# Optimization experiments

Measured on AMD Instinct MI355X. Metric: run time of the kernel, lower is better.

## Reference

```python
import jax, jax.numpy as jnp
import numpy as np

B, N, H_DIM, E_DIM, M_DIM = 16, 128, 128, 64, 128


def setup_inputs() -> dict:
    key = jax.random.key(0)
    k_h, k_e, k_adj, k_w, k_b = jax.random.split(key, 5)
    h = jax.random.normal(k_h, (B, N, H_DIM), dtype=jnp.float32)
    e = jax.random.normal(k_e, (B, N, N, E_DIM), dtype=jnp.float32)
    # binary adjacency mask stored as float (multiplied elementwise, as in torch)
    adj = (jax.random.uniform(k_adj, (B, N, N)) < 0.3).astype(jnp.float32)
    in_dim = 2 * H_DIM + E_DIM
    # nn.Linear default init: U(-1/sqrt(fan_in), 1/sqrt(fan_in))
    bound = 1.0 / np.sqrt(in_dim)
    W = jax.random.uniform(k_w, (in_dim, M_DIM), minval=-bound, maxval=bound, dtype=jnp.float32)
    b = jax.random.uniform(k_b, (M_DIM,), minval=-bound, maxval=bound, dtype=jnp.float32)
    return {"h": h, "e": e, "adj": adj, "W": W, "b": b}


def reference(h, e, adj, W, b):
    # torch: cat([h_j (unsqueeze(1) repeat), h_i (unsqueeze(2) repeat), e], -1) @ W + b, then * adj
    # Split the concat-linear into three matmuls (same math, no O(N^2 * (2h+e)) cat tensor):
    hd = h.shape[-1]
    W1 = W[:hd]          # acts on h_repeat_1 = h[b, j]
    W2 = W[hd:2 * hd]    # acts on h_repeat_2 = h[b, i]
    W3 = W[2 * hd:]      # acts on e[b, i, j]
    t1 = jnp.einsum('bjd,dm->bjm', h, W1)[:, None, :, :]   # broadcast over i
    t2 = jnp.einsum('bid,dm->bim', h, W2)[:, :, None, :]   # broadcast over j
    t3 = jnp.einsum('bije,em->bijm', e, W3)
    m = (t1 + t2 + t3 + b) * adj[..., None]                 # [B, N, N, M_DIM]
    return m
```

## Files before the change

### kernel.cpp

```cpp
#include <hip/hip_runtime.h>
#include <hip/hip_bf16.h>

#define NB 16
#define NN 128
#define HD 128
#define ED 64
#define MD 128

typedef float f32x4 __attribute__((ext_vector_type(4)));

__global__ __launch_bounds__(128, 8) void prep_kernel(
    const float* __restrict__ h, const float* __restrict__ W,
    const float* __restrict__ bias,
    float* __restrict__ hw1, float* __restrict__ t2pb)
{
    __shared__ float hs[HD];
    const int row = blockIdx.x;
    const int m   = threadIdx.x;

    hs[m] = h[(size_t)row * HD + m];
    __syncthreads();

    float a1 = 0.f, a2 = 0.f;
    const float* W1p = W + m;
    const float* W2p = W + (size_t)HD * MD + m;
#pragma unroll 8
    for (int d = 0; d < HD; ++d) {
        const float hv = hs[d];
        a1 = fmaf(hv, W1p[(size_t)d * MD], a1);
        a2 = fmaf(hv, W2p[(size_t)d * MD], a2);
    }
    hw1 [(size_t)row * MD + m] = a1;
    t2pb[(size_t)row * MD + m] = a2 + bias[m];
}

__global__ __launch_bounds__(512, 4) void msg_kernel(
    const float* __restrict__ e, const float* __restrict__ adj,
    const float* __restrict__ W, const float* __restrict__ hw1,
    const float* __restrict__ t2pb, float* __restrict__ out)
{
    __shared__ float smem[16384];
    float4* __restrict__ eq = (float4*)smem;
    float4* __restrict__ wq = (float4*)(smem + 8192);

    const int bx   = blockIdx.x;
    const int tid  = threadIdx.x;
    const int w    = __builtin_amdgcn_readfirstlane(tid >> 6);
    const int lane = tid & 63;

    const float4* __restrict__ e4  = (const float4*)(e + (size_t)bx * NN * ED);
    const float4* __restrict__ W3q = (const float4*)(W + (size_t)(2 * HD) * MD);

#pragma unroll
    for (int it = 0; it < 4; ++it) {
        const int idx = tid + it * 512;
        const int j   = idx >> 4;
        const int kq  = idx & 15;
        eq[16 * j + (kq ^ (j & 7))] = e4[idx];
        wq[idx] = W3q[idx];
    }
    __syncthreads();

    const int jhalf = w & 1;
    const int mq4   = w >> 1;
    const int j     = jhalf * 64 + lane;
    const int jx    = j & 7;
    const int ebase = 16 * j;
    const int wbase = 8 * mq4;

    float acc[32];
#pragma unroll
    for (int i = 0; i < 32; ++i) acc[i] = 0.f;

#pragma unroll 2
    for (int q = 0; q < 16; ++q) {
        const float4 ev = eq[ebase + (q ^ jx)];
#pragma unroll
        for (int kk = 0; kk < 4; ++kk) {
            const float evk = (kk == 0) ? ev.x : (kk == 1) ? ev.y
                             : (kk == 2) ? ev.z : ev.w;
            const float4* __restrict__ wrow = wq + 32 * (4 * q + kk) + wbase;
#pragma unroll
            for (int p = 0; p < 8; ++p) {
                const float4 wv = wrow[p];
                acc[4 * p + 0] = fmaf(evk, wv.x, acc[4 * p + 0]);
                acc[4 * p + 1] = fmaf(evk, wv.y, acc[4 * p + 1]);
                acc[4 * p + 2] = fmaf(evk, wv.z, acc[4 * p + 2]);
                acc[4 * p + 3] = fmaf(evk, wv.w, acc[4 * p + 3]);
            }
        }
    }

    float4* __restrict__ tq = wq;
    const float*  __restrict__ adjrow = adj  + (size_t)bx * NN;
    const float4* __restrict__ hw1b   = (const float4*)(hw1 + (size_t)(bx >> 7) * NN * MD);
    const float4* __restrict__ t2row  = (const float4*)(t2pb + (size_t)bx * MD);
    f32x4*        __restrict__ outb   = (f32x4*)(out + (size_t)bx * NN * MD);

#pragma unroll
    for (int h = 0; h < 2; ++h) {
        __syncthreads();
        if (jhalf == h) {
            const int lx = lane & 7;
#pragma unroll
            for (int p = 0; p < 8; ++p) {
                const int qm = wbase + p;
                tq[32 * lane + (qm ^ lx)] =
                    make_float4(acc[4 * p + 0], acc[4 * p + 1],
                                acc[4 * p + 2], acc[4 * p + 3]);
            }
        }
        __syncthreads();
#pragma unroll
        for (int it = 0; it < 4; ++it) {
            const int t4 = tid + it * 512;
            const int jl = t4 >> 5;
            const int mq = t4 & 31;
            const int jg = h * 64 + jl;
            const float4 v  = tq[32 * jl + (mq ^ (jl & 7))];
            const float4 h1 = hw1b[(size_t)jg * 32 + mq];
            const float4 t2 = t2row[mq];
            const float  a  = adjrow[jg];
            f32x4 r;
            r.x = (v.x + h1.x + t2.x) * a;
            r.y = (v.y + h1.y + t2.y) * a;
            r.z = (v.z + h1.z + t2.z) * a;
            r.w = (v.w + h1.w + t2.w) * a;
            __builtin_nontemporal_store(r, outb + (size_t)jg * 32 + mq);
        }
    }
}

extern "C" void kernel_launch(void* const* d_in, const int* in_sizes, int n_in,
                              void* d_out, int out_size, void* d_ws, size_t ws_size,
                              hipStream_t stream)
{
    const float* h    = (const float*)d_in[0];
    const float* e    = (const float*)d_in[1];
    const float* adj  = (const float*)d_in[2];
    const float* W    = (const float*)d_in[3];
    const float* bias = (const float*)d_in[4];
    float* out = (float*)d_out;

    float* hw1  = (float*)d_ws;
    float* t2pb = hw1 + (size_t)NB * NN * MD;

    prep_kernel<<<dim3(NB * NN), dim3(128), 0, stream>>>(h, W, bias, hw1, t2pb);
    msg_kernel <<<dim3(NB * NN), dim3(512), 0, stream>>>(e, adj, W, hw1, t2pb, out);
}
```

Measured before the change: 239.0 us.

## Halve block size, register-block two j rows per thread, load e directly from global

The message kernel now runs 256 threads per block. Each thread accumulates two j rows (j and j+64) and reuses each LDS W3 read across both. The e tile is no longer staged in shared memory: each thread reads its float4s straight from global, which cuts LDS to 32 KB and the W3 read traffic per FMA. The cost is 64 accumulators per thread, raising register pressure and possibly occupancy limits, plus strided uncoalesced global loads of e.

Result: no change. 239.4 us (+0.2%).

```diff
diff --git a/kernel.cpp b/kernel.cpp
--- a/kernel.cpp
+++ b/kernel.cpp
@@ -34,14 +34,12 @@
     t2pb[(size_t)row * MD + m] = a2 + bias[m];
 }
 
-__global__ __launch_bounds__(512, 4) void msg_kernel(
+__global__ __launch_bounds__(256, 4) void msg_kernel(
     const float* __restrict__ e, const float* __restrict__ adj,
     const float* __restrict__ W, const float* __restrict__ hw1,
     const float* __restrict__ t2pb, float* __restrict__ out)
 {
-    __shared__ float smem[16384];
-    float4* __restrict__ eq = (float4*)smem;
-    float4* __restrict__ wq = (float4*)(smem + 8192);
+    __shared__ float4 smem[2048];
 
     const int bx   = blockIdx.x;
     const int tid  = threadIdx.x;
@@ -52,46 +50,45 @@
     const float4* __restrict__ W3q = (const float4*)(W + (size_t)(2 * HD) * MD);
 
 #pragma unroll
-    for (int it = 0; it < 4; ++it) {
-        const int idx = tid + it * 512;
-        const int j   = idx >> 4;
-        const int kq  = idx & 15;
-        eq[16 * j + (kq ^ (j & 7))] = e4[idx];
-        wq[idx] = W3q[idx];
-    }
+    for (int it = 0; it < 8; ++it)
+        smem[tid + it * 256] = W3q[tid + it * 256];
     __syncthreads();
 
-    const int jhalf = w & 1;
-    const int mq4   = w >> 1;
-    const int j     = jhalf * 64 + lane;
-    const int jx    = j & 7;
-    const int ebase = 16 * j;
-    const int wbase = 8 * mq4;
+    const int wbase = 8 * w;
 
-    float acc[32];
+    float acc[2][32];
 #pragma unroll
-    for (int i = 0; i < 32; ++i) acc[i] = 0.f;
+    for (int r = 0; r < 2; ++r)
+#pragma unroll
+        for (int i = 0; i < 32; ++i) acc[r][i] = 0.f;
 
 #pragma unroll 2
     for (int q = 0; q < 16; ++q) {
-        const float4 ev = eq[ebase + (q ^ jx)];
+        const float4 ev0 = e4[lane * 16 + q];
+        const float4 ev1 = e4[(lane + 64) * 16 + q];
 #pragma unroll
         for (int kk = 0; kk < 4; ++kk) {
-            const float evk = (kk == 0) ? ev.x : (kk == 1) ? ev.y
-                             : (kk == 2) ? ev.z : ev.w;
-            const float4* __restrict__ wrow = wq + 32 * (4 * q + kk) + wbase;
+            const float e0 = (kk == 0) ? ev0.x : (kk == 1) ? ev0.y
+                            : (kk == 2) ? ev0.z : ev0.w;
+            const float e1 = (kk == 0) ? ev1.x : (kk == 1) ? ev1.y
+                            : (kk == 2) ? ev1.z : ev1.w;
+            const float4* __restrict__ wrow = smem + 32 * (4 * q + kk) + wbase;
 #pragma unroll
             for (int p = 0; p < 8; ++p) {
                 const float4 wv = wrow[p];
-                acc[4 * p + 0] = fmaf(evk, wv.x, acc[4 * p + 0]);
-                acc[4 * p + 1] = fmaf(evk, wv.y, acc[4 * p + 1]);
-                acc[4 * p + 2] = fmaf(evk, wv.z, acc[4 * p + 2]);
-                acc[4 * p + 3] = fmaf(evk, wv.w, acc[4 * p + 3]);
+                acc[0][4 * p + 0] = fmaf(e0, wv.x, acc[0][4 * p + 0]);
+                acc[0][4 * p + 1] = fmaf(e0, wv.y, acc[0][4 * p + 1]);
+                acc[0][4 * p + 2] = fmaf(e0, wv.z, acc[0][4 * p + 2]);
+                acc[0][4 * p + 3] = fmaf(e0, wv.w, acc[0][4 * p + 3]);
+                acc[1][4 * p + 0] = fmaf(e1, wv.x, acc[1][4 * p + 0]);
+                acc[1][4 * p + 1] = fmaf(e1, wv.y, acc[1][4 * p + 1]);
+                acc[1][4 * p + 2] = fmaf(e1, wv.z, acc[1][4 * p + 2]);
+                acc[1][4 * p + 3] = fmaf(e1, wv.w, acc[1][4 * p + 3]);
             }
         }
     }
 
-    float4* __restrict__ tq = wq;
+    float4* __restrict__ tq = smem;
     const float*  __restrict__ adjrow = adj  + (size_t)bx * NN;
     const float4* __restrict__ hw1b   = (const float4*)(hw1 + (size_t)(bx >> 7) * NN * MD);
     const float4* __restrict__ t2row  = (const float4*)(t2pb + (size_t)bx * MD);
@@ -100,20 +97,20 @@
 #pragma unroll
     for (int h = 0; h < 2; ++h) {
         __syncthreads();
-        if (jhalf == h) {
+        {
             const int lx = lane & 7;
 #pragma unroll
             for (int p = 0; p < 8; ++p) {
                 const int qm = wbase + p;
                 tq[32 * lane + (qm ^ lx)] =
-                    make_float4(acc[4 * p + 0], acc[4 * p + 1],
-                                acc[4 * p + 2], acc[4 * p + 3]);
+                    make_float4(acc[h][4 * p + 0], acc[h][4 * p + 1],
+                                acc[h][4 * p + 2], acc[h][4 * p + 3]);
             }
         }
         __syncthreads();
 #pragma unroll
-        for (int it = 0; it < 4; ++it) {
-            const int t4 = tid + it * 512;
+        for (int it = 0; it < 8; ++it) {
+            const int t4 = tid + it * 256;
             const int jl = t4 >> 5;
             const int mq = t4 & 31;
             const int jg = h * 64 + jl;
@@ -146,5 +143,5 @@
     float* t2pb = hw1 + (size_t)NB * NN * MD;
 
     prep_kernel<<<dim3(NB * NN), dim3(128), 0, stream>>>(h, W, bias, hw1, t2pb);
-    msg_kernel <<<dim3(NB * NN), dim3(512), 0, stream>>>(e, adj, W, hw1, t2pb, out);
+    msg_kernel <<<dim3(NB * NN), dim3(256), 0, stream>>>(e, adj, W, hw1, t2pb, out);
 }
```

## Compute edge projection with split-bf16 MFMA instead of scalar FP32 FMAs

Applied to the files above, without the earlier changes.

The e@W3 product per (b,i) row is moved from scalar FP32 FMAs onto bf16 MFMA instructions. Each FP32 operand is split into a high and a low bf16 part, and three MFMA passes (hi*hi, hi*lo, lo*hi) approximate FP32 accuracy. Half the waves load and pack W3 into LDS while the other half load and pack e, and the epilogue now writes the full tile to LDS once instead of in two halves. The trade-off is that W3 is re-packed in every block and there is some precision loss from dropping the lo*lo term.

After: 209.4 us. -12.4%, faster.

```diff
diff --git a/kernel.cpp b/kernel.cpp
--- a/kernel.cpp
+++ b/kernel.cpp
@@ -8,6 +8,16 @@
 #define MD 128
 
 typedef float f32x4 __attribute__((ext_vector_type(4)));
+typedef short bf16x8 __attribute__((ext_vector_type(8)));
+
+__device__ __forceinline__ unsigned pack_hi(float a, float b) {
+    return (__float_as_uint(a) >> 16) | (__float_as_uint(b) & 0xFFFF0000u);
+}
+__device__ __forceinline__ unsigned pack_lo(float a, float b) {
+    const float ra = a - __uint_as_float(__float_as_uint(a) & 0xFFFF0000u);
+    const float rb = b - __uint_as_float(__float_as_uint(b) & 0xFFFF0000u);
+    return (__float_as_uint(ra) >> 16) | (__float_as_uint(rb) & 0xFFFF0000u);
+}
 
 __global__ __launch_bounds__(128, 8) void prep_kernel(
     const float* __restrict__ h, const float* __restrict__ W,
@@ -39,95 +49,148 @@
     const float* __restrict__ W, const float* __restrict__ hw1,
     const float* __restrict__ t2pb, float* __restrict__ out)
 {
-    __shared__ float smem[16384];
-    float4* __restrict__ eq = (float4*)smem;
-    float4* __restrict__ wq = (float4*)(smem + 8192);
+    __shared__ char smem[65536];
 
     const int bx   = blockIdx.x;
     const int tid  = threadIdx.x;
+    const int lane = tid & 63;
     const int w    = __builtin_amdgcn_readfirstlane(tid >> 6);
-    const int lane = tid & 63;
-
-    const float4* __restrict__ e4  = (const float4*)(e + (size_t)bx * NN * ED);
-    const float4* __restrict__ W3q = (const float4*)(W + (size_t)(2 * HD) * MD);
-
-#pragma unroll
-    for (int it = 0; it < 4; ++it) {
-        const int idx = tid + it * 512;
-        const int j   = idx >> 4;
-        const int kq  = idx & 15;
-        eq[16 * j + (kq ^ (j & 7))] = e4[idx];
-        wq[idx] = W3q[idx];
-    }
-    __syncthreads();
-
-    const int jhalf = w & 1;
-    const int mq4   = w >> 1;
-    const int j     = jhalf * 64 + lane;
-    const int jx    = j & 7;
-    const int ebase = 16 * j;
-    const int wbase = 8 * mq4;
-
-    float acc[32];
-#pragma unroll
-    for (int i = 0; i < 32; ++i) acc[i] = 0.f;
-
-#pragma unroll 2
-    for (int q = 0; q < 16; ++q) {
-        const float4 ev = eq[ebase + (q ^ jx)];
-#pragma unroll
-        for (int kk = 0; kk < 4; ++kk) {
-            const float evk = (kk == 0) ? ev.x : (kk == 1) ? ev.y
-                             : (kk == 2) ? ev.z : ev.w;
-            const float4* __restrict__ wrow = wq + 32 * (4 * q + kk) + wbase;
-#pragma unroll
-            for (int p = 0; p < 8; ++p) {
-                const float4 wv = wrow[p];
-                acc[4 * p + 0] = fmaf(evk, wv.x, acc[4 * p + 0]);
-                acc[4 * p + 1] = fmaf(evk, wv.y, acc[4 * p + 1]);
-                acc[4 * p + 2] = fmaf(evk, wv.z, acc[4 * p + 2]);
-                acc[4 * p + 3] = fmaf(evk, wv.w, acc[4 * p + 3]);
+
+    if (w < 4) {
+        const int m  = tid & 127;
+        const int kh = tid >> 7;
+        const float* __restrict__ W3 = W + (size_t)(2 * HD) * MD;
+        float col[32];
+#pragma unroll
+        for (int k = 0; k < 32; ++k)
+            col[k] = W3[(size_t)(kh * 32 + k) * MD + m];
+        const unsigned swz = (unsigned)((m & 7) << 4);
+#pragma unroll
+        for (int q = 0; q < 4; ++q) {
+            uint4 hi, lo;
+            hi.x = pack_hi(col[8*q+0], col[8*q+1]);
+            hi.y = pack_hi(col[8*q+2], col[8*q+3]);
+            hi.z = pack_hi(col[8*q+4], col[8*q+5]);
+            hi.w = pack_hi(col[8*q+6], col[8*q+7]);
+            lo.x = pack_lo(col[8*q+0], col[8*q+1]);
+            lo.y = pack_lo(col[8*q+2], col[8*q+3]);
+            lo.z = pack_lo(col[8*q+4], col[8*q+5]);
+            lo.w = pack_lo(col[8*q+6], col[8*q+7]);
+            const unsigned off = (unsigned)((m << 7) + (kh << 6) + (q << 4)) ^ swz;
+            *(uint4*)(smem + 32768 + off) = hi;
+            *(uint4*)(smem + 49152 + off) = lo;
+        }
+    } else {
+        const int s = tid - 256;
+        const float4* __restrict__ e4 = (const float4*)(e + (size_t)bx * NN * ED);
+        float4 ev[8];
+#pragma unroll
+        for (int it = 0; it < 8; ++it)
+            ev[it] = e4[it * 256 + s];
+#pragma unroll
+        for (int it = 0; it < 8; ++it) {
+            const int idx = it * 256 + s;
+            const int j   = idx >> 4;
+            const int kq  = idx & 15;
+            const unsigned off =
+                ((unsigned)((j << 7) + (kq << 3))) ^ (unsigned)((j & 7) << 4);
+            uint2 hi, lo;
+            hi.x = pack_hi(ev[it].x, ev[it].y);
+            hi.y = pack_hi(ev[it].z, ev[it].w);
+            lo.x = pack_lo(ev[it].x, ev[it].y);
+            lo.y = pack_lo(ev[it].z, ev[it].w);
+            *(uint2*)(smem + off)         = hi;
+            *(uint2*)(smem + 16384 + off) = lo;
+        }
+    }
+    __syncthreads();
+
+    const int jh  = w & 1;
+    const int mq  = w >> 1;
+    const int jb  = jh * 64;
+    const int mb  = mq * 32;
+    const int l15 = lane & 15;
+    const int g   = lane >> 4;
+
+    f32x4 acc[4][2];
+#pragma unroll
+    for (int jt = 0; jt < 4; ++jt)
+#pragma unroll
+        for (int mt = 0; mt < 2; ++mt)
+            acc[jt][mt] = (f32x4){0.f, 0.f, 0.f, 0.f};
+
+#pragma unroll
+    for (int pass = 0; pass < 3; ++pass) {
+        const int abase = (pass == 2) ? 16384 : 0;
+        const int bbase = (pass == 1) ? 49152 : 32768;
+#pragma unroll
+        for (int kt = 0; kt < 2; ++kt) {
+            bf16x8 a[4], b[2];
+#pragma unroll
+            for (int jt = 0; jt < 4; ++jt) {
+                const int j = jb + jt * 16 + l15;
+                const unsigned off =
+                    ((unsigned)((j << 7) + (kt << 6) + (g << 4)))
+                    ^ (unsigned)((j & 7) << 4);
+                a[jt] = *(const bf16x8*)(smem + abase + off);
             }
-        }
-    }
-
-    float4* __restrict__ tq = wq;
+#pragma unroll
+            for (int mt = 0; mt < 2; ++mt) {
+                const int mm = mb + mt * 16 + l15;
+                const unsigned off =
+                    ((unsigned)((mm << 7) + (kt << 6) + (g << 4)))
+                    ^ (unsigned)((mm & 7) << 4);
+                b[mt] = *(const bf16x8*)(smem + bbase + off);
+            }
+#pragma unroll
+            for (int jt = 0; jt < 4; ++jt)
+#pragma unroll
+                for (int mt = 0; mt < 2; ++mt)
+                    acc[jt][mt] = __builtin_amdgcn_mfma_f32_16x16x32_bf16(
+                        a[jt], b[mt], acc[jt][mt], 0, 0, 0);
+        }
+    }
+    __syncthreads();
+
+#pragma unroll
+    for (int jt = 0; jt < 4; ++jt) {
+#pragma unroll
+        for (int mt = 0; mt < 2; ++mt) {
+#pragma unroll
+            for (int r = 0; r < 4; ++r) {
+                const int j  = jb + jt * 16 + g * 4 + r;
+                const int mm = mb + mt * 16 + l15;
+                const unsigned off =
+                    ((unsigned)((j << 9) + (mm << 2)))
+                    ^ (unsigned)((j & 7) << 4);
+                *(float*)(smem + off) = acc[jt][mt][r];
+            }
+        }
+    }
+    __syncthreads();
+
     const float*  __restrict__ adjrow = adj  + (size_t)bx * NN;
     const float4* __restrict__ hw1b   = (const float4*)(hw1 + (size_t)(bx >> 7) * NN * MD);
     const float4* __restrict__ t2row  = (const float4*)(t2pb + (size_t)bx * MD);
     f32x4*        __restrict__ outb   = (f32x4*)(out + (size_t)bx * NN * MD);
 
 #pragma unroll
-    for (int h = 0; h < 2; ++h) {
-        __syncthreads();
-        if (jhalf == h) {
-            const int lx = lane & 7;
-#pragma unroll
-            for (int p = 0; p < 8; ++p) {
-                const int qm = wbase + p;
-                tq[32 * lane + (qm ^ lx)] =
-                    make_float4(acc[4 * p + 0], acc[4 * p + 1],
-                                acc[4 * p + 2], acc[4 * p + 3]);
-            }
-        }
-        __syncthreads();
-#pragma unroll
-        for (int it = 0; it < 4; ++it) {
-            const int t4 = tid + it * 512;
-            const int jl = t4 >> 5;
-            const int mq = t4 & 31;
-            const int jg = h * 64 + jl;
-            const float4 v  = tq[32 * jl + (mq ^ (jl & 7))];
-            const float4 h1 = hw1b[(size_t)jg * 32 + mq];
-            const float4 t2 = t2row[mq];
-            const float  a  = adjrow[jg];
-            f32x4 r;
-            r.x = (v.x + h1.x + t2.x) * a;
-            r.y = (v.y + h1.y + t2.y) * a;
-            r.z = (v.z + h1.z + t2.z) * a;
-            r.w = (v.w + h1.w + t2.w) * a;
-            __builtin_nontemporal_store(r, outb + (size_t)jg * 32 + mq);
-        }
+    for (int it = 0; it < 8; ++it) {
+        const int t4 = tid + it * 512;
+        const int j  = t4 >> 5;
+        const int q  = t4 & 31;
+        const unsigned off =
+            ((unsigned)((j << 9) + (q << 4))) ^ (unsigned)((j & 7) << 4);
+        const float4 v  = *(const float4*)(smem + off);
+        const float4 h1 = hw1b[(size_t)j * 32 + q];
+        const float4 t2 = t2row[q];
+        const float  a  = adjrow[j];
+        f32x4 r;
+        r.x = (v.x + h1.x + t2.x) * a;
+        r.y = (v.y + h1.y + t2.y) * a;
+        r.z = (v.z + h1.z + t2.z) * a;
+        r.w = (v.w + h1.w + t2.w) * a;
+        __builtin_nontemporal_store(r, outb + (size_t)j * 32 + q);
     }
 }
 
```
